# Performance work log

Hardware: AMD Instinct MI355X
Metric: run time of the kernel (lower is better)

Reference implementation:

```python
import jax, jax.numpy as jnp
import numpy as np

N = 50000      # nodes
E = 800000     # edges (avg degree 16)
DIN = 256      # input_dim
H = 4          # heads
C = 32         # output_dim per head
HID = H * C    # 128
NEG_SLOPE = 0.2


def setup_inputs() -> dict:
    key = jax.random.key(0)
    ks = jax.random.split(key, 12)
    s = 0.05
    d = {}
    d["x"] = jax.random.normal(ks[0], (N, DIN), jnp.float32)
    d["edge_index"] = jax.random.randint(ks[1], (2, E), 0, N, jnp.int32)
    # GATv2Conv layer 0 (in=DIN)
    d["Wl0"] = jax.random.normal(ks[2], (HID, DIN), jnp.float32) * s
    d["Wr0"] = jax.random.normal(ks[3], (HID, DIN), jnp.float32) * s
    d["att0"] = jax.random.normal(ks[4], (H, C), jnp.float32) * s
    d["b0"] = jnp.zeros((HID,), jnp.float32)
    # GATv2Conv layer 1 (in=HID)
    d["Wl1"] = jax.random.normal(ks[5], (HID, HID), jnp.float32) * s
    d["Wr1"] = jax.random.normal(ks[6], (HID, HID), jnp.float32) * s
    d["att1"] = jax.random.normal(ks[7], (H, C), jnp.float32) * s
    d["b1"] = jnp.zeros((HID,), jnp.float32)
    # down_proj: Linear(HID -> C)
    d["down_W"] = jax.random.normal(ks[8], (C, HID), jnp.float32) * s
    d["down_b"] = jnp.zeros((C,), jnp.float32)
    return d


def _gatv2_layer(x, src, dst, Wl, Wr, att, b, n):
    # x: [n, Din]; src/dst: [Etot] (self loops included)
    xl = (x @ Wl.T).reshape(n, H, C)   # messages (x_j side, lin_l)
    xr = (x @ Wr.T).reshape(n, H, C)   # target side (x_i, lin_r)
    e = jax.nn.leaky_relu(xl[src] + xr[dst], NEG_SLOPE)   # [Etot, H, C]
    logits = jnp.einsum('ehc,hc->eh', e, att)             # [Etot, H]
    # softmax over incoming edges per destination node
    m = jax.ops.segment_max(logits, dst, num_segments=n)
    ex = jnp.exp(logits - m[dst])
    den = jax.ops.segment_sum(ex, dst, num_segments=n)
    alpha = ex / den[dst]                                 # [Etot, H]
    out = jax.ops.segment_sum(alpha[:, :, None] * xl[src], dst, num_segments=n)
    return out.reshape(n, HID) + b                        # concat heads + bias


def reference(x, edge_index, Wl0, Wr0, att0, b0, Wl1, Wr1, att1, b1, down_W, down_b):
    n = x.shape[0]
    loops = jnp.arange(n, dtype=edge_index.dtype)
    ei = jnp.concatenate([edge_index, jnp.stack([loops, loops])], axis=1)  # add_self_loops=True
    src, dst = ei[0], ei[1]
    h = _gatv2_layer(x, src, dst, Wl0, Wr0, att0, b0, n)
    h = _gatv2_layer(h, src, dst, Wl1, Wr1, att1, b1, n)
    return h @ down_W.T + down_b    # down_proj: [n, C]
```

## Files before the change

kernel.cpp:

```cpp
#include <hip/hip_runtime.h>

#define CAP 64
#define BCAP 6144

typedef _Float16 h8 __attribute__((ext_vector_type(8)));
typedef _Float16 h4 __attribute__((ext_vector_type(4)));
typedef _Float16 h2 __attribute__((ext_vector_type(2)));
typedef float f32x4 __attribute__((ext_vector_type(4)));

__device__ __forceinline__ uint4 pack8(float4 a, float4 b){
  union { h8 h; uint4 u; } cv;
  cv.h = (h8){ (_Float16)a.x, (_Float16)a.y, (_Float16)a.z, (_Float16)a.w,
               (_Float16)b.x, (_Float16)b.y, (_Float16)b.z, (_Float16)b.w };
  return cv.u;
}

__device__ __forceinline__ float edge_logit(uint4 xu, const h2* xrh, const h2* avh){
  union { uint4 u; h2 v[4]; } cu; cu.u = xu;
  const h2 z2 = { (_Float16)0.f, (_Float16)0.f };
  const h2 sl = { (_Float16)0.2f, (_Float16)0.2f };
  float p = 0.f;
  #pragma unroll
  for (int k = 0; k < 4; ++k){
    h2 t  = cu.v[k] + xrh[k];
    h2 hi = __builtin_elementwise_max(t, z2);
    h2 lo = __builtin_elementwise_min(t, z2);
    h2 lr = hi + lo * sl;
    p = __builtin_amdgcn_fdot2(lr, avh[k], p, false);
  }
  return p;
}
__device__ __forceinline__ void acc_edge(float w, uint4 xu, float* accv){
  union { uint4 u; _Float16 e[8]; } ce; ce.u = xu;
  #pragma unroll
  for (int i = 0; i < 8; ++i) accv[i] += w * (float)ce.e[i];
}

__device__ __forceinline__ void tile_map(int gi, int nby, int& bx, int& by){
  const int nby8 = nby & ~7;
  if (gi < 2 * nby8){
    int g8 = gi >> 4, r = gi & 15;
    bx = r >> 3;
    by = g8 * 8 + (r & 7);
  } else {
    int t = gi - 2 * nby8, rem = nby - nby8;
    bx = t / rem;
    by = nby8 + t % rem;
  }
}

__global__ void convw_kernel(const float* __restrict__ Wl0, const float* __restrict__ Wr0,
                             const float* __restrict__ Wl1, const float* __restrict__ Wr1,
                             _Float16* __restrict__ B0h, _Float16* __restrict__ B1h){
  int t = blockIdx.x * blockDim.x + threadIdx.x;
  const float* s; _Float16* d; int off;
  if (t < 8192)      { s = Wl0; d = B0h;          off = t; }
  else if (t < 16384){ s = Wr0; d = B0h + 32768;  off = t - 8192; }
  else if (t < 20480){ s = Wl1; d = B1h;          off = t - 16384; }
  else               { s = Wr1; d = B1h + 16384;  off = t - 20480; }
  float4 f = ((const float4*)s)[off];
  h4 h = { (_Float16)f.x, (_Float16)f.y, (_Float16)f.z, (_Float16)f.w };
  *(h4*)(d + 4 * (size_t)off) = h;
}

__global__ void scatter_kernel(const int* __restrict__ cnt, const int* __restrict__ hist,
                               int* __restrict__ cursor, int* __restrict__ perm, int n){
  __shared__ int base[64];
  __shared__ int lh[64];
  __shared__ int lbase[64];
  __shared__ int ht[64];
  if (threadIdx.x < 64){
    lh[threadIdx.x] = 0;
    ht[threadIdx.x] = hist[threadIdx.x];
  }
  __syncthreads();
  if (threadIdx.x == 0){
    int acc = 0;
    for (int d = 63; d >= 0; --d){ base[d] = acc; acc += ht[d]; }
  }
  int i = blockIdx.x * blockDim.x + threadIdx.x;
  int d = 1, lr = 0;
  if (i < n){
    d = cnt[i]; d = (d < 1) ? 1 : (d > CAP ? CAP : d);
    lr = atomicAdd(&lh[d - 1], 1);
  }
  __syncthreads();
  if (threadIdx.x < 64 && lh[threadIdx.x] > 0)
    lbase[threadIdx.x] = atomicAdd(&cursor[threadIdx.x], lh[threadIdx.x]);
  __syncthreads();
  if (i < n)
    perm[base[d - 1] + lbase[d - 1] + lr] = i;
}

__device__ __forceinline__ void gemm_body(
    char* smem, const float* __restrict__ A32, const _Float16* __restrict__ A16,
    const _Float16* __restrict__ Bw, _Float16* __restrict__ C, int n, int K,
    int bx, int by)
{
  char* Abase = smem;
  char* Bbase = smem + 8192;

  const int tid  = threadIdx.x;
  const int lane = tid & 63;
  const int wx   = tid >> 6;
  const int r0   = by * 64;
  const int cb   = bx * 128;
  const int m16  = lane & 15, quad = lane >> 4;

  f32x4 acc[4][2];
  #pragma unroll
  for (int i = 0; i < 4; ++i)
    #pragma unroll
    for (int j = 0; j < 2; ++j)
      acc[i][j] = (f32x4){0.f, 0.f, 0.f, 0.f};

  const int srow = tid >> 2;
  const int kq   = (tid & 3) << 4;
  const int kb   = kq * 2;
  const int swz  = (srow & 7) << 4;

  uint4 ra[2], rb[2][2];
  const uint4 z = {0u, 0u, 0u, 0u};

  if (r0 + srow < n){
    if (A32){
      const float* p = A32 + (size_t)(r0 + srow) * K + kq;
      ra[0] = pack8(*(const float4*)(p),     *(const float4*)(p + 4));
      ra[1] = pack8(*(const float4*)(p + 8), *(const float4*)(p + 12));
    } else {
      const _Float16* p = A16 + (size_t)(r0 + srow) * K + kq;
      ra[0] = *(const uint4*)(p);
      ra[1] = *(const uint4*)(p + 8);
    }
  } else { ra[0] = z; ra[1] = z; }
  #pragma unroll
  for (int v = 0; v < 2; ++v){
    const _Float16* p = Bw + (size_t)(cb + v * 64 + srow) * K + kq;
    rb[v][0] = *(const uint4*)(p);
    rb[v][1] = *(const uint4*)(p + 8);
  }

  const int nt = K >> 6;
  for (int t = 0; t < nt; ++t){
    *(uint4*)(Abase + srow * 128 + (kb ^ swz))        = ra[0];
    *(uint4*)(Abase + srow * 128 + ((kb + 16) ^ swz)) = ra[1];
    #pragma unroll
    for (int v = 0; v < 2; ++v){
      *(uint4*)(Bbase + (v * 64 + srow) * 128 + (kb ^ swz))        = rb[v][0];
      *(uint4*)(Bbase + (v * 64 + srow) * 128 + ((kb + 16) ^ swz)) = rb[v][1];
    }
    __syncthreads();
    if (t + 1 < nt){
      int kt = (t + 1) << 6;
      if (r0 + srow < n){
        if (A32){
          const float* p = A32 + (size_t)(r0 + srow) * K + kt + kq;
          ra[0] = pack8(*(const float4*)(p),     *(const float4*)(p + 4));
          ra[1] = pack8(*(const float4*)(p + 8), *(const float4*)(p + 12));
        } else {
          const _Float16* p = A16 + (size_t)(r0 + srow) * K + kt + kq;
          ra[0] = *(const uint4*)(p);
          ra[1] = *(const uint4*)(p + 8);
        }
      }
      #pragma unroll
      for (int v = 0; v < 2; ++v){
        const _Float16* p = Bw + (size_t)(cb + v * 64 + srow) * K + kt + kq;
        rb[v][0] = *(const uint4*)(p);
        rb[v][1] = *(const uint4*)(p + 8);
      }
    }
    const int swr = (m16 & 7) << 4;
    #pragma unroll
    for (int ks = 0; ks < 2; ++ks){
      const int k0 = ks * 32 + quad * 8;
      const int cbyte = (k0 * 2) ^ swr;
      h8 a[4], b[2];
      #pragma unroll
      for (int i = 0; i < 4; ++i)
        a[i] = *(const h8*)(Abase + (i * 16 + m16) * 128 + cbyte);
      #pragma unroll
      for (int j = 0; j < 2; ++j)
        b[j] = *(const h8*)(Bbase + (wx * 32 + j * 16 + m16) * 128 + cbyte);
      #pragma unroll
      for (int i = 0; i < 4; ++i)
        #pragma unroll
        for (int j = 0; j < 2; ++j)
          acc[i][j] = __builtin_amdgcn_mfma_f32_16x16x32_f16(a[i], b[j], acc[i][j], 0, 0, 0);
    }
    __syncthreads();
  }

  _Float16* Csm = (_Float16*)smem;
  #pragma unroll
  for (int i = 0; i < 4; ++i)
    #pragma unroll
    for (int r = 0; r < 4; ++r){
      int lrow = i * 16 + quad * 4 + r;
      _Float16* cp = Csm + lrow * 136 + wx * 32 + m16;
      #pragma unroll
      for (int j = 0; j < 2; ++j)
        cp[j * 16] = (_Float16)acc[i][j][r];
    }
  __syncthreads();
  #pragma unroll
  for (int v = 0; v < 4; ++v){
    int idx = v * 256 + tid;
    int row = idx >> 4, cx = (idx & 15) * 8;
    if (r0 + row < n)
      *(uint4*)(C + (size_t)(r0 + row) * 256 + cb + cx)
        = *(const uint4*)(Csm + row * 136 + cx);
  }
}

__global__ __launch_bounds__(256) void gemm_mfma(
    const float* __restrict__ A32, const _Float16* __restrict__ A16,
    const _Float16* __restrict__ Bw, _Float16* __restrict__ C, int n, int K)
{
  __shared__ __align__(16) char smem[24576];
  const int nby = (n + 63) / 64;
  int bx, by;
  tile_map(blockIdx.x, nby, bx, by);
  gemm_body(smem, A32, A16, Bw, C, n, K, bx, by);
}

__global__ __launch_bounds__(256) void gemm_pass1(
    const float* __restrict__ A32, const _Float16* __restrict__ Bw,
    _Float16* __restrict__ C, int n,
    const int* __restrict__ ei, int* __restrict__ bins, int* __restrict__ bcursor,
    int e_orig, int etot, int NP)
{
  __shared__ __align__(16) char smem[24576];
  const int lin = blockIdx.x;
  if (lin >= NP){
    const int nby = (n + 63) / 64;
    int bx, by;
    tile_map(lin - NP, nby, bx, by);
    gemm_body(smem, A32, nullptr, Bw, C, n, 256, bx, by);
  } else {
    int* lcnt  = (int*)smem;
    int* gbase = lcnt + 256;
    const int tid = threadIdx.x;
    if (tid < 196) lcnt[tid] = 0;
    __syncthreads();
    const int base = lin * 2048 + tid;
    int pk[8], bk[8], lp[8];
    #pragma unroll
    for (int k = 0; k < 8; ++k){
      int i = base + k * 256;
      bk[k] = -1;
      if (i < etot){
        int src, dst;
        if (i < e_orig){ src = ei[i]; dst = ei[e_orig + i]; }
        else { src = i - e_orig; dst = src; }
        bk[k] = dst >> 8;
        pk[k] = ((dst & 255) << 24) | src;
      }
    }
    #pragma unroll
    for (int k = 0; k < 8; ++k)
      if (bk[k] >= 0) lp[k] = atomicAdd(&lcnt[bk[k]], 1);
    __syncthreads();
    if (tid < 196 && lcnt[tid] > 0)
      gbase[tid] = atomicAdd(&bcursor[tid], lcnt[tid]);
    __syncthreads();
    #pragma unroll
    for (int k = 0; k < 8; ++k)
      if (bk[k] >= 0){
        int p = gbase[bk[k]] + lp[k];
        if (p < BCAP) bins[(size_t)bk[k] * BCAP + p] = pk[k];
      }
  }
}

__global__ __launch_bounds__(256) void pass2_kernel(
    const int* __restrict__ bins, const int* __restrict__ bcursor,
    int* __restrict__ cnt, int* __restrict__ col2, int* __restrict__ hist, int n)
{
  __shared__ int stage[256 * CAP];
  __shared__ int lcnt2[256];
  __shared__ int lh[64];
  const int b = blockIdx.x, tid = threadIdx.x;
  lcnt2[tid] = 0;
  if (tid < 64) lh[tid] = 0;
  __syncthreads();
  int ecnt = bcursor[b]; if (ecnt > BCAP) ecnt = BCAP;
  for (int i = tid; i < ecnt; i += 256){
    int v = bins[(size_t)b * BCAP + i];
    int src = v & 0xFFFFFF;
    int loc = ((unsigned)v) >> 24;
    int pos = atomicAdd(&lcnt2[loc], 1);
    if (pos < CAP) stage[loc * CAP + pos] = src;
  }
  __syncthreads();
  int node = b * 256 + tid;
  if (node < n){
    int d = lcnt2[tid];
    cnt[node] = d;
    int dc = d < 1 ? 1 : (d > CAP ? CAP : d);
    atomicAdd(&lh[dc - 1], 1);
  }
  __syncthreads();
  const uint4* sg = (const uint4*)stage;
  uint4* c4 = (uint4*)col2;
  for (int k2 = tid; k2 < 4096; k2 += 256){
    int nd = b * 256 + (k2 >> 4);
    if (nd < n) c4[(size_t)nd * 16 + (k2 & 15)] = sg[k2];
  }
  if (tid < 64 && lh[tid] > 0) atomicAdd(&hist[tid], lh[tid]);
}

__global__ __launch_bounds__(128) void agg_wave(
    const _Float16* __restrict__ XLR, const int* __restrict__ col2,
    const int* __restrict__ cnt, const int* __restrict__ perm,
    const float* __restrict__ att,
    const float* __restrict__ bias, _Float16* __restrict__ H16, int n)
{
  __shared__ int idxs[8][72];
  const int lane  = threadIdx.x & 63;
  const int g     = lane >> 4;
  const int ll    = lane & 15;
  const int gbase = g << 4;
  const int nl    = ((threadIdx.x >> 6) << 2) + g;
  const int slot  = blockIdx.x * 8 + nl;
  if (slot >= n) return;
  const int node = perm[slot];
  int deg = cnt[node]; if (deg > CAP) deg = CAP;
  const int c0 = 8 * ll;

  h2 xrh[4], avh[4];
  {
    union { uint4 u; h2 v[4]; } xc;
    xc.u = *(const uint4*)(XLR + (size_t)node * 256 + 128 + c0);
    #pragma unroll
    for (int k = 0; k < 4; ++k) xrh[k] = xc.v[k];
    #pragma unroll
    for (int k = 0; k < 4; ++k)
      avh[k] = (h2){ (_Float16)att[c0 + 2*k], (_Float16)att[c0 + 2*k + 1] };
  }

  {
    int sq[4];
    #pragma unroll
    for (int q = 0; q < 4; ++q)
      sq[q] = (ll + 16*q < deg) ? col2[(size_t)node * CAP + ll + 16*q] : 0;
    int s0 = __shfl(sq[0], gbase);
    #pragma unroll
    for (int q = 0; q < 4; ++q)
      idxs[nl][ll + 16*q] = (ll + 16*q < deg) ? sq[q] : s0;
    if (ll < 8) idxs[nl][64 + ll] = s0;
  }
  const int* idxp = idxs[nl];

  float l = 0.f, accv[8];
  #pragma unroll
  for (int i = 0; i < 8; ++i) accv[i] = 0.f;

  uint4 x0, x1, x2, x3, x4, x5, x6, x7;
  {
    int e0 = idxp[0], e1 = idxp[1], e2 = idxp[2], e3 = idxp[3];
    int e4 = idxp[4], e5 = idxp[5], e6 = idxp[6], e7 = idxp[7];
    x0 = *(const uint4*)(XLR + (size_t)e0 * 256 + c0);
    x1 = *(const uint4*)(XLR + (size_t)e1 * 256 + c0);
    x2 = *(const uint4*)(XLR + (size_t)e2 * 256 + c0);
    x3 = *(const uint4*)(XLR + (size_t)e3 * 256 + c0);
    x4 = *(const uint4*)(XLR + (size_t)e4 * 256 + c0);
    x5 = *(const uint4*)(XLR + (size_t)e5 * 256 + c0);
    x6 = *(const uint4*)(XLR + (size_t)e6 * 256 + c0);
    x7 = *(const uint4*)(XLR + (size_t)e7 * 256 + c0);
  }

  int j = 0;
  for (; j + 4 <= deg; j += 4){
    uint4 y0 = x0, y1 = x1, y2 = x2, y3 = x3;
    x0 = x4; x1 = x5; x2 = x6; x3 = x7;
    int e8  = idxp[j + 8],  e9  = idxp[j + 9];
    int e10 = idxp[j + 10], e11 = idxp[j + 11];
    x4 = *(const uint4*)(XLR + (size_t)e8  * 256 + c0);
    x5 = *(const uint4*)(XLR + (size_t)e9  * 256 + c0);
    x6 = *(const uint4*)(XLR + (size_t)e10 * 256 + c0);
    x7 = *(const uint4*)(XLR + (size_t)e11 * 256 + c0);
    float p0 = edge_logit(y0, xrh, avh);
    float p1 = edge_logit(y1, xrh, avh);
    float p2 = edge_logit(y2, xrh, avh);
    float p3 = edge_logit(y3, xrh, avh);
    p0 += __shfl_xor(p0, 1);  p1 += __shfl_xor(p1, 1);
    p2 += __shfl_xor(p2, 1);  p3 += __shfl_xor(p3, 1);
    p0 += __shfl_xor(p0, 2);  p1 += __shfl_xor(p1, 2);
    p2 += __shfl_xor(p2, 2);  p3 += __shfl_xor(p3, 2);
    float w0 = __expf(p0), w1 = __expf(p1), w2 = __expf(p2), w3 = __expf(p3);
    l += (w0 + w1) + (w2 + w3);
    acc_edge(w0, y0, accv); acc_edge(w1, y1, accv);
    acc_edge(w2, y2, accv); acc_edge(w3, y3, accv);
  }
  #pragma unroll
  for (int r = 0; r < 3; ++r){
    if (j + r < deg){
      uint4 xe = (r == 0) ? x0 : ((r == 1) ? x1 : x2);
      float p = edge_logit(xe, xrh, avh);
      p += __shfl_xor(p, 1);
      p += __shfl_xor(p, 2);
      float w = __expf(p);
      l += w;
      acc_edge(w, xe, accv);
    }
  }
  float inv = 1.f / l;
  union { h8 h; uint4 u; } o;
  #pragma unroll
  for (int i = 0; i < 8; ++i)
    o.h[i] = (_Float16)(accv[i] * inv + bias[c0 + i]);
  *(uint4*)(H16 + (size_t)node * 128 + c0) = o.u;
}

__global__ __launch_bounds__(256) void agg_down(
    const _Float16* __restrict__ XLR, const int* __restrict__ col2,
    const int* __restrict__ cnt, const int* __restrict__ perm,
    const float* __restrict__ att,
    const float* __restrict__ bias, const float* __restrict__ dW,
    const float* __restrict__ db, float* __restrict__ out, int n)
{
  __shared__ float dwb[32][129];
  __shared__ float hsm[16][128];
  __shared__ int idxs[16][72];
  for (int i = threadIdx.x; i < 32 * 128; i += 256)
    dwb[i >> 7][i & 127] = dW[i];

  const int lane  = threadIdx.x & 63;
  const int g     = lane >> 4;
  const int ll    = lane & 15;
  const int gbase = g << 4;
  const int nl    = ((threadIdx.x >> 6) << 2) + g;
  const int slot  = blockIdx.x * 16 + nl;
  const bool valid = slot < n;
  const int node = valid ? perm[slot] : 0;
  int deg = 0;
  if (valid){ deg = cnt[node]; if (deg > CAP) deg = CAP; }
  const int c0 = 8 * ll;

  h2 xrh[4], avh[4];
  {
    union { uint4 u; h2 v[4]; } xc;
    xc.u = (uint4){0u,0u,0u,0u};
    if (valid) xc.u = *(const uint4*)(XLR + (size_t)node * 256 + 128 + c0);
    #pragma unroll
    for (int k = 0; k < 4; ++k) xrh[k] = xc.v[k];
    #pragma unroll
    for (int k = 0; k < 4; ++k)
      avh[k] = (h2){ (_Float16)att[c0 + 2*k], (_Float16)att[c0 + 2*k + 1] };
  }

  {
    int sq[4];
    #pragma unroll
    for (int q = 0; q < 4; ++q)
      sq[q] = (valid && ll + 16*q < deg) ? col2[(size_t)node * CAP + ll + 16*q] : 0;
    int s0 = __shfl(sq[0], gbase);
    #pragma unroll
    for (int q = 0; q < 4; ++q)
      idxs[nl][ll + 16*q] = (ll + 16*q < deg) ? sq[q] : s0;
    if (ll < 8) idxs[nl][64 + ll] = s0;
  }
  const int* idxp = idxs[nl];

  float l = 0.f, accv[8];
  #pragma unroll
  for (int i = 0; i < 8; ++i) accv[i] = 0.f;

  uint4 x0, x1, x2, x3, x4, x5, x6, x7;
  {
    int e0 = idxp[0], e1 = idxp[1], e2 = idxp[2], e3 = idxp[3];
    int e4 = idxp[4], e5 = idxp[5], e6 = idxp[6], e7 = idxp[7];
    x0 = *(const uint4*)(XLR + (size_t)e0 * 256 + c0);
    x1 = *(const uint4*)(XLR + (size_t)e1 * 256 + c0);
    x2 = *(const uint4*)(XLR + (size_t)e2 * 256 + c0);
    x3 = *(const uint4*)(XLR + (size_t)e3 * 256 + c0);
    x4 = *(const uint4*)(XLR + (size_t)e4 * 256 + c0);
    x5 = *(const uint4*)(XLR + (size_t)e5 * 256 + c0);
    x6 = *(const uint4*)(XLR + (size_t)e6 * 256 + c0);
    x7 = *(const uint4*)(XLR + (size_t)e7 * 256 + c0);
  }

  int j = 0;
  for (; j + 4 <= deg; j += 4){
    uint4 y0 = x0, y1 = x1, y2 = x2, y3 = x3;
    x0 = x4; x1 = x5; x2 = x6; x3 = x7;
    int e8  = idxp[j + 8],  e9  = idxp[j + 9];
    int e10 = idxp[j + 10], e11 = idxp[j + 11];
    x4 = *(const uint4*)(XLR + (size_t)e8  * 256 + c0);
    x5 = *(const uint4*)(XLR + (size_t)e9  * 256 + c0);
    x6 = *(const uint4*)(XLR + (size_t)e10 * 256 + c0);
    x7 = *(const uint4*)(XLR + (size_t)e11 * 256 + c0);
    float p0 = edge_logit(y0, xrh, avh);
    float p1 = edge_logit(y1, xrh, avh);
    float p2 = edge_logit(y2, xrh, avh);
    float p3 = edge_logit(y3, xrh, avh);
    p0 += __shfl_xor(p0, 1);  p1 += __shfl_xor(p1, 1);
    p2 += __shfl_xor(p2, 1);  p3 += __shfl_xor(p3, 1);
    p0 += __shfl_xor(p0, 2);  p1 += __shfl_xor(p1, 2);
    p2 += __shfl_xor(p2, 2);  p3 += __shfl_xor(p3, 2);
    float w0 = __expf(p0), w1 = __expf(p1), w2 = __expf(p2), w3 = __expf(p3);
    l += (w0 + w1) + (w2 + w3);
    acc_edge(w0, y0, accv); acc_edge(w1, y1, accv);
    acc_edge(w2, y2, accv); acc_edge(w3, y3, accv);
  }
  #pragma unroll
  for (int r = 0; r < 3; ++r){
    if (j + r < deg){
      uint4 xe = (r == 0) ? x0 : ((r == 1) ? x1 : x2);
      float p = edge_logit(xe, xrh, avh);
      p += __shfl_xor(p, 1);
      p += __shfl_xor(p, 2);
      float w = __expf(p);
      l += w;
      acc_edge(w, xe, accv);
    }
  }
  {
    float inv = (deg > 0) ? 1.f / l : 0.f;
    #pragma unroll
    for (int i = 0; i < 8; ++i)
      hsm[nl][c0 + i] = accv[i] * inv + bias[c0 + i];
  }
  __syncthreads();

  const int o = threadIdx.x & 31;
  #pragma unroll
  for (int h2i = 0; h2i < 2; ++h2i){
    int nl2 = (threadIdx.x >> 5) + h2i * 8;
    int slot2 = blockIdx.x * 16 + nl2;
    float sum = 0.f;
    #pragma unroll 8
    for (int k = 0; k < 128; ++k)
      sum += hsm[nl2][k] * dwb[o][k];
    if (slot2 < n)
      out[(size_t)perm[slot2] * 32 + o] = sum + db[o];
  }
}

extern "C" void kernel_launch(void* const* d_in, const int* in_sizes, int n_in,
                              void* d_out, int out_size, void* d_ws, size_t ws_size,
                              hipStream_t stream) {
  const float* x     = (const float*)d_in[0];
  const int*   ei    = (const int*)  d_in[1];
  const float* Wl0   = (const float*)d_in[2];
  const float* Wr0   = (const float*)d_in[3];
  const float* att0  = (const float*)d_in[4];
  const float* b0    = (const float*)d_in[5];
  const float* Wl1   = (const float*)d_in[6];
  const float* Wr1   = (const float*)d_in[7];
  const float* att1  = (const float*)d_in[8];
  const float* b1    = (const float*)d_in[9];
  const float* dW    = (const float*)d_in[10];
  const float* db    = (const float*)d_in[11];
  float* out = (float*)d_out;

  const int n    = in_sizes[0] / 256;
  const int e    = in_sizes[1] / 2;
  const int etot = e + n;

  _Float16* XLR16 = (_Float16*)d_ws;
  _Float16* H16   = XLR16 + (size_t)n * 256;
  int* col2 = (int*)(H16 + (size_t)n * 128);
  int* cnt  = col2 + (size_t)n * CAP;
  int* hist    = cnt + n;
  int* cursor  = hist + 64;
  int* bcursor = cursor + 64;
  int* perm    = bcursor + 256;
  _Float16* B0h = (_Float16*)(perm + ((n + 3) & ~3));
  _Float16* B1h = B0h + 65536;
  int* bins = (int*)H16;

  (void)hipMemsetAsync(cnt, 0, ((size_t)n + 384) * sizeof(int), stream);
  convw_kernel<<<96, 256, 0, stream>>>(Wl0, Wr0, Wl1, Wr1, B0h, B1h);

  const int NP = (etot + 2047) / 2048;
  const int NG = 2 * ((n + 63) / 64);
  gemm_pass1<<<NP + NG, 256, 0, stream>>>(x, B0h, XLR16, n, ei, bins, bcursor,
                                          e, etot, NP);

  const int NB2 = (n + 255) / 256;
  pass2_kernel<<<NB2, 256, 0, stream>>>(bins, bcursor, cnt, col2, hist, n);
  scatter_kernel<<<(n + 255) / 256, 256, 0, stream>>>(cnt, hist, cursor, perm, n);

  agg_wave<<<(n + 7) / 8, 128, 0, stream>>>(XLR16, col2, cnt, perm, att0, b0, H16, n);
  gemm_mfma<<<NG, 256, 0, stream>>>(nullptr, H16, B1h, XLR16, n, 128);
  agg_down<<<(n + 15) / 16, 256, 0, stream>>>(XLR16, col2, cnt, perm, att1, b1, dW, db, out, n);
}
```

Before: 270.7 us.

## Fold weight conversion and degree sort into existing kernels, drop two launches

The layer-0 GEMM now reads fp32 weights directly and converts them in registers, and the layer-1 weight conversion runs as extra blocks of the fused pass1 kernel, so the separate convert kernel goes away. The global degree histogram and scatter kernel are replaced by a per-block local degree sort inside pass2, which writes perm with -1 padding. The aggregation kernels skip padded slots. Two kernel launches and a large memset are removed, at the cost of degree sorting only within 256-node blocks and extra fp32 weight loads in the GEMM.

```diff
diff --git a/kernel.cpp b/kernel.cpp
--- a/kernel.cpp
+++ b/kernel.cpp
@@ -49,53 +49,10 @@
   }
 }
 
-__global__ void convw_kernel(const float* __restrict__ Wl0, const float* __restrict__ Wr0,
-                             const float* __restrict__ Wl1, const float* __restrict__ Wr1,
-                             _Float16* __restrict__ B0h, _Float16* __restrict__ B1h){
-  int t = blockIdx.x * blockDim.x + threadIdx.x;
-  const float* s; _Float16* d; int off;
-  if (t < 8192)      { s = Wl0; d = B0h;          off = t; }
-  else if (t < 16384){ s = Wr0; d = B0h + 32768;  off = t - 8192; }
-  else if (t < 20480){ s = Wl1; d = B1h;          off = t - 16384; }
-  else               { s = Wr1; d = B1h + 16384;  off = t - 20480; }
-  float4 f = ((const float4*)s)[off];
-  h4 h = { (_Float16)f.x, (_Float16)f.y, (_Float16)f.z, (_Float16)f.w };
-  *(h4*)(d + 4 * (size_t)off) = h;
-}
-
-__global__ void scatter_kernel(const int* __restrict__ cnt, const int* __restrict__ hist,
-                               int* __restrict__ cursor, int* __restrict__ perm, int n){
-  __shared__ int base[64];
-  __shared__ int lh[64];
-  __shared__ int lbase[64];
-  __shared__ int ht[64];
-  if (threadIdx.x < 64){
-    lh[threadIdx.x] = 0;
-    ht[threadIdx.x] = hist[threadIdx.x];
-  }
-  __syncthreads();
-  if (threadIdx.x == 0){
-    int acc = 0;
-    for (int d = 63; d >= 0; --d){ base[d] = acc; acc += ht[d]; }
-  }
-  int i = blockIdx.x * blockDim.x + threadIdx.x;
-  int d = 1, lr = 0;
-  if (i < n){
-    d = cnt[i]; d = (d < 1) ? 1 : (d > CAP ? CAP : d);
-    lr = atomicAdd(&lh[d - 1], 1);
-  }
-  __syncthreads();
-  if (threadIdx.x < 64 && lh[threadIdx.x] > 0)
-    lbase[threadIdx.x] = atomicAdd(&cursor[threadIdx.x], lh[threadIdx.x]);
-  __syncthreads();
-  if (i < n)
-    perm[base[d - 1] + lbase[d - 1] + lr] = i;
-}
-
 __device__ __forceinline__ void gemm_body(
     char* smem, const float* __restrict__ A32, const _Float16* __restrict__ A16,
-    const _Float16* __restrict__ Bw, _Float16* __restrict__ C, int n, int K,
-    int bx, int by)
+    const float* __restrict__ B32, const _Float16* __restrict__ Bw,
+    _Float16* __restrict__ C, int n, int K, int bx, int by)
 {
   char* Abase = smem;
   char* Bbase = smem + 8192;
@@ -135,9 +92,15 @@
   } else { ra[0] = z; ra[1] = z; }
   #pragma unroll
   for (int v = 0; v < 2; ++v){
-    const _Float16* p = Bw + (size_t)(cb + v * 64 + srow) * K + kq;
-    rb[v][0] = *(const uint4*)(p);
-    rb[v][1] = *(const uint4*)(p + 8);
+    if (B32){
+      const float* p = B32 + (size_t)(v * 64 + srow) * K + kq;
+      rb[v][0] = pack8(*(const float4*)(p),     *(const float4*)(p + 4));
+      rb[v][1] = pack8(*(const float4*)(p + 8), *(const float4*)(p + 12));
+    } else {
+      const _Float16* p = Bw + (size_t)(cb + v * 64 + srow) * K + kq;
+      rb[v][0] = *(const uint4*)(p);
+      rb[v][1] = *(const uint4*)(p + 8);
+    }
   }
 
   const int nt = K >> 6;
@@ -165,9 +128,15 @@
       }
       #pragma unroll
       for (int v = 0; v < 2; ++v){
-        const _Float16* p = Bw + (size_t)(cb + v * 64 + srow) * K + kt + kq;
-        rb[v][0] = *(const uint4*)(p);
-        rb[v][1] = *(const uint4*)(p + 8);
+        if (B32){
+          const float* p = B32 + (size_t)(v * 64 + srow) * K + kt + kq;
+          rb[v][0] = pack8(*(const float4*)(p),     *(const float4*)(p + 4));
+          rb[v][1] = pack8(*(const float4*)(p + 8), *(const float4*)(p + 12));
+        } else {
+          const _Float16* p = Bw + (size_t)(cb + v * 64 + srow) * K + kt + kq;
+          rb[v][0] = *(const uint4*)(p);
+          rb[v][1] = *(const uint4*)(p + 8);
+        }
       }
     }
     const int swr = (m16 & 7) << 4;
@@ -214,29 +183,39 @@
 }
 
 __global__ __launch_bounds__(256) void gemm_mfma(
-    const float* __restrict__ A32, const _Float16* __restrict__ A16,
-    const _Float16* __restrict__ Bw, _Float16* __restrict__ C, int n, int K)
+    const _Float16* __restrict__ A16, const _Float16* __restrict__ Bw,
+    _Float16* __restrict__ C, int n, int K)
 {
   __shared__ __align__(16) char smem[24576];
   const int nby = (n + 63) / 64;
   int bx, by;
   tile_map(blockIdx.x, nby, bx, by);
-  gemm_body(smem, A32, A16, Bw, C, n, K, bx, by);
+  gemm_body(smem, nullptr, A16, nullptr, Bw, C, n, K, bx, by);
 }
 
 __global__ __launch_bounds__(256) void gemm_pass1(
-    const float* __restrict__ A32, const _Float16* __restrict__ Bw,
-    _Float16* __restrict__ C, int n,
+    const float* __restrict__ A32,
+    const float* __restrict__ Wl0, const float* __restrict__ Wr0,
+    const float* __restrict__ Wl1, const float* __restrict__ Wr1,
+    _Float16* __restrict__ B1h, _Float16* __restrict__ C, int n,
     const int* __restrict__ ei, int* __restrict__ bins, int* __restrict__ bcursor,
     int e_orig, int etot, int NP)
 {
   __shared__ __align__(16) char smem[24576];
   const int lin = blockIdx.x;
-  if (lin >= NP){
+  if (lin >= NP + 32){
     const int nby = (n + 63) / 64;
     int bx, by;
-    tile_map(lin - NP, nby, bx, by);
-    gemm_body(smem, A32, nullptr, Bw, C, n, 256, bx, by);
+    tile_map(lin - NP - 32, nby, bx, by);
+    gemm_body(smem, A32, nullptr, (bx == 0) ? Wl0 : Wr0, nullptr, C, n, 256, bx, by);
+  } else if (lin >= NP){
+    int t = (lin - NP) * 256 + (int)threadIdx.x;
+    const float* s; _Float16* d; int off;
+    if (t < 4096){ s = Wl1; d = B1h;         off = t; }
+    else         { s = Wr1; d = B1h + 16384; off = t - 4096; }
+    float4 f = ((const float4*)s)[off];
+    h4 h = { (_Float16)f.x, (_Float16)f.y, (_Float16)f.z, (_Float16)f.w };
+    *(h4*)(d + 4 * (size_t)off) = h;
   } else {
     int* lcnt  = (int*)smem;
     int* gbase = lcnt + 256;
@@ -275,14 +254,14 @@
 
 __global__ __launch_bounds__(256) void pass2_kernel(
     const int* __restrict__ bins, const int* __restrict__ bcursor,
-    int* __restrict__ cnt, int* __restrict__ col2, int* __restrict__ hist, int n)
+    int* __restrict__ cnt, int* __restrict__ col2, int* __restrict__ perm, int n)
 {
   __shared__ int stage[256 * CAP];
   __shared__ int lcnt2[256];
-  __shared__ int lh[64];
+  __shared__ int dh[64], dbase[64], dcur[64];
   const int b = blockIdx.x, tid = threadIdx.x;
   lcnt2[tid] = 0;
-  if (tid < 64) lh[tid] = 0;
+  if (tid < 64){ dh[tid] = 0; dcur[tid] = 0; }
   __syncthreads();
   int ecnt = bcursor[b]; if (ecnt > BCAP) ecnt = BCAP;
   for (int i = tid; i < ecnt; i += 256){
@@ -292,29 +271,39 @@
     int pos = atomicAdd(&lcnt2[loc], 1);
     if (pos < CAP) stage[loc * CAP + pos] = src;
   }
+  perm[b * 256 + tid] = -1;
   __syncthreads();
-  int node = b * 256 + tid;
+  const int node = b * 256 + tid;
+  int dc = 1;
   if (node < n){
     int d = lcnt2[tid];
     cnt[node] = d;
-    int dc = d < 1 ? 1 : (d > CAP ? CAP : d);
-    atomicAdd(&lh[dc - 1], 1);
+    dc = d < 1 ? 1 : (d > CAP ? CAP : d);
+    atomicAdd(&dh[dc - 1], 1);
   }
   __syncthreads();
+  if (tid == 0){
+    int acc = 0;
+    for (int k = 63; k >= 0; --k){ dbase[k] = acc; acc += dh[k]; }
+  }
+  __syncthreads();
+  if (node < n){
+    int rank = dbase[dc - 1] + atomicAdd(&dcur[dc - 1], 1);
+    perm[b * 256 + rank] = node;
+  }
   const uint4* sg = (const uint4*)stage;
   uint4* c4 = (uint4*)col2;
   for (int k2 = tid; k2 < 4096; k2 += 256){
     int nd = b * 256 + (k2 >> 4);
     if (nd < n) c4[(size_t)nd * 16 + (k2 & 15)] = sg[k2];
   }
-  if (tid < 64 && lh[tid] > 0) atomicAdd(&hist[tid], lh[tid]);
 }
 
 __global__ __launch_bounds__(128) void agg_wave(
     const _Float16* __restrict__ XLR, const int* __restrict__ col2,
     const int* __restrict__ cnt, const int* __restrict__ perm,
     const float* __restrict__ att,
-    const float* __restrict__ bias, _Float16* __restrict__ H16, int n)
+    const float* __restrict__ bias, _Float16* __restrict__ H16, int nslot)
 {
   __shared__ int idxs[8][72];
   const int lane  = threadIdx.x & 63;
@@ -323,8 +312,9 @@
   const int gbase = g << 4;
   const int nl    = ((threadIdx.x >> 6) << 2) + g;
   const int slot  = blockIdx.x * 8 + nl;
-  if (slot >= n) return;
+  if (slot >= nslot) return;
   const int node = perm[slot];
+  if (node < 0) return;
   int deg = cnt[node]; if (deg > CAP) deg = CAP;
   const int c0 = 8 * ll;
 
@@ -418,7 +408,7 @@
     const int* __restrict__ cnt, const int* __restrict__ perm,
     const float* __restrict__ att,
     const float* __restrict__ bias, const float* __restrict__ dW,
-    const float* __restrict__ db, float* __restrict__ out, int n)
+    const float* __restrict__ db, float* __restrict__ out, int nslot)
 {
   __shared__ float dwb[32][129];
   __shared__ float hsm[16][128];
@@ -432,8 +422,9 @@
   const int gbase = g << 4;
   const int nl    = ((threadIdx.x >> 6) << 2) + g;
   const int slot  = blockIdx.x * 16 + nl;
-  const bool valid = slot < n;
-  const int node = valid ? perm[slot] : 0;
+  int node = (slot < nslot) ? perm[slot] : -1;
+  const bool valid = node >= 0;
+  node = valid ? node : 0;
   int deg = 0;
   if (valid){ deg = cnt[node]; if (deg > CAP) deg = CAP; }
   const int c0 = 8 * ll;
@@ -529,12 +520,13 @@
   for (int h2i = 0; h2i < 2; ++h2i){
     int nl2 = (threadIdx.x >> 5) + h2i * 8;
     int slot2 = blockIdx.x * 16 + nl2;
+    int n2 = (slot2 < nslot) ? perm[slot2] : -1;
     float sum = 0.f;
     #pragma unroll 8
     for (int k = 0; k < 128; ++k)
       sum += hsm[nl2][k] * dwb[o][k];
-    if (slot2 < n)
-      out[(size_t)perm[slot2] * 32 + o] = sum + db[o];
+    if (n2 >= 0)
+      out[(size_t)n2 * 32 + o] = sum + db[o];
   }
 }
 
@@ -559,31 +551,30 @@
   const int e    = in_sizes[1] / 2;
   const int etot = e + n;
 
+  const int NB2   = (n + 255) / 256;
+  const int NSLOT = NB2 * 256;
+
   _Float16* XLR16 = (_Float16*)d_ws;
   _Float16* H16   = XLR16 + (size_t)n * 256;
   int* col2 = (int*)(H16 + (size_t)n * 128);
   int* cnt  = col2 + (size_t)n * CAP;
-  int* hist    = cnt + n;
-  int* cursor  = hist + 64;
-  int* bcursor = cursor + 64;
+  int* bcursor = cnt + n;
   int* perm    = bcursor + 256;
-  _Float16* B0h = (_Float16*)(perm + ((n + 3) & ~3));
-  _Float16* B1h = B0h + 65536;
+  _Float16* B1h = (_Float16*)(perm + NSLOT);
   int* bins = (int*)H16;
 
-  (void)hipMemsetAsync(cnt, 0, ((size_t)n + 384) * sizeof(int), stream);
-  convw_kernel<<<96, 256, 0, stream>>>(Wl0, Wr0, Wl1, Wr1, B0h, B1h);
+  (void)hipMemsetAsync(bcursor, 0, 256 * sizeof(int), stream);
 
   const int NP = (etot + 2047) / 2048;
   const int NG = 2 * ((n + 63) / 64);
-  gemm_pass1<<<NP + NG, 256, 0, stream>>>(x, B0h, XLR16, n, ei, bins, bcursor,
-                                          e, etot, NP);
-
-  const int NB2 = (n + 255) / 256;
-  pass2_kernel<<<NB2, 256, 0, stream>>>(bins, bcursor, cnt, col2, hist, n);
-  scatter_kernel<<<(n + 255) / 256, 256, 0, stream>>>(cnt, hist, cursor, perm, n);
-
-  agg_wave<<<(n + 7) / 8, 128, 0, stream>>>(XLR16, col2, cnt, perm, att0, b0, H16, n);
-  gemm_mfma<<<NG, 256, 0, stream>>>(nullptr, H16, B1h, XLR16, n, 128);
-  agg_down<<<(n + 15) / 16, 256, 0, stream>>>(XLR16, col2, cnt, perm, att1, b1, dW, db, out, n);
-}
+  gemm_pass1<<<NP + 32 + NG, 256, 0, stream>>>(x, Wl0, Wr0, Wl1, Wr1, B1h,
+                                               XLR16, n, ei, bins, bcursor,
+                                               e, etot, NP);
+
+  pass2_kernel<<<NB2, 256, 0, stream>>>(bins, bcursor, cnt, col2, perm, n);
+
+  agg_wave<<<NSLOT / 8, 128, 0, stream>>>(XLR16, col2, cnt, perm, att0, b0, H16, NSLOT);
+  gemm_mfma<<<NG, 256, 0, stream>>>(H16, B1h, XLR16, n, 128);
+  agg_down<<<NSLOT / 16, 256, 0, stream>>>(XLR16, col2, cnt, perm, att1, b1,
+                                           dW, db, out, NSLOT);
+}
```

New measurement: 250.6 us. -7.4%, faster.
